# Kernel tuning notes

Measured on AMD Instinct MI355X. Metric: run time of the kernel, lower is better.

The kernel has to match this reference:

```python
import jax, jax.numpy as jnp
import numpy as np

N_HEAD = 16
NEG = -1e30  # finite stand-in for -inf; keeps softmax NaN-free


def setup_inputs() -> dict:
    key = jax.random.key(0)
    k1, k2, k3, k4, k5, k6 = jax.random.split(key, 6)
    B, T, C = 4, 2048, 1024
    x = jax.random.normal(k1, (B, T, C), dtype=jnp.float32)
    # realistic right-padding: True = padded position
    lengths = jax.random.randint(k2, (B,), T // 2, T + 1)  # at least half valid
    padding_mask = jnp.arange(T)[None, :] >= lengths[:, None]  # [B,T] bool
    s = 0.02
    W_attn = jax.random.normal(k3, (C, 3 * C), dtype=jnp.float32) * s
    b_attn = jnp.zeros((3 * C,), dtype=jnp.float32)
    W_proj = jax.random.normal(k4, (C, C), dtype=jnp.float32) * s
    b_proj = jnp.zeros((C,), dtype=jnp.float32)
    return {"x": x, "padding_mask": padding_mask, "W_attn": W_attn,
            "b_attn": b_attn, "W_proj": W_proj, "b_proj": b_proj}


def reference(x, padding_mask, W_attn, b_attn, W_proj, b_proj):
    B, T, C = x.shape
    H, D = N_HEAD, C // N_HEAD
    qkv = x @ W_attn + b_attn  # [B,T,3C]
    q, k, v = jnp.split(qkv, 3, axis=-1)
    q = q.reshape(B, T, H, D).transpose(0, 2, 1, 3)  # [B,H,T,D]
    k = k.reshape(B, T, H, D).transpose(0, 2, 1, 3)
    v = v.reshape(B, T, H, D).transpose(0, 2, 1, 3)
    att = jnp.einsum('bhqd,bhkd->bhqk', q, k) / jnp.sqrt(jnp.float32(D))
    causal = jnp.tril(jnp.ones((T, T), dtype=bool))  # [T,T]
    invalid = padding_mask[:, None, None, :] | ~causal[None, None]  # [B,1,T,T] key invalid
    att = jnp.where(invalid, NEG, att)
    att = jax.nn.softmax(att, axis=-1)
    # rows where every key is masked: torch softmax gives NaN -> nan_to_num(0)
    any_valid = jnp.any(~invalid, axis=-1, keepdims=True)  # [B,1,T,1]
    att = jnp.where(any_valid, att, 0.0)
    y = jnp.einsum('bhqk,bhkd->bhqd', att, v)  # [B,H,T,D]
    y = y.transpose(0, 2, 1, 3).reshape(B, T, C)
    y = y @ W_proj + b_proj
    y = jnp.where(padding_mask[:, :, None], 0.0, y)
    return y
```

## Files before the change

### kernel.cpp

```cpp
#include <hip/hip_runtime.h>
#include <stdint.h>

#define T_SEQ 2048
#define CDIM  1024
#define NH    16
#define DH    64
#define BATCH 4
#define MROWS (BATCH * T_SEQ)
#define N3    (3 * CDIM)
#define NEGBIG -1e30f

typedef unsigned short u16;
typedef __attribute__((ext_vector_type(8))) __bf16 bf16x8;
typedef __attribute__((ext_vector_type(4))) __bf16 bf16x4;
typedef __attribute__((ext_vector_type(8))) unsigned short u16x8;
typedef __attribute__((ext_vector_type(4))) float f32x4;
typedef __attribute__((ext_vector_type(16))) float f32x16;
typedef __attribute__((ext_vector_type(4))) unsigned int u32x4;

__device__ inline u16 f2bf(float f) {
  uint32_t u = __builtin_bit_cast(uint32_t, f);
  u += 0x7FFFu + ((u >> 16) & 1u);
  return (u16)(u >> 16);
}

__device__ inline void gld_lds16(const void* g, void* l) {
  __builtin_amdgcn_global_load_lds(
      (const __attribute__((address_space(1))) void*)g,
      (__attribute__((address_space(3))) void*)l, 16, 0, 0);
}


__global__ __launch_bounds__(256) void cvt_f32_bf16(
    const float* __restrict__ in, u16* __restrict__ out, int n) {
  int i = (blockIdx.x * 256 + threadIdx.x) * 4;
  if (i >= n) return;
  float4 v = *(const float4*)&in[i];
  ushort4 o; o.x = f2bf(v.x); o.y = f2bf(v.y); o.z = f2bf(v.z); o.w = f2bf(v.w);
  *(ushort4*)&out[i] = o;
}

__global__ __launch_bounds__(256) void wt_tiled(
    const float* __restrict__ W, u16* __restrict__ WT, int K, int N) {
  __shared__ float tile[64][65];
  const int k0 = blockIdx.y * 64, n0 = blockIdx.x * 64;
  const int t = threadIdx.x, cr = t >> 6, cc = t & 63;
#pragma unroll
  for (int i = 0; i < 16; i++) {
    int r = i * 4 + cr;
    tile[r][cc] = W[(size_t)(k0 + r) * N + n0 + cc];
  }
  __syncthreads();
#pragma unroll
  for (int i = 0; i < 16; i++) {
    int r = i * 4 + cr;
    WT[(size_t)(n0 + r) * K + k0 + cc] = f2bf(tile[cc][r]);
  }
}

__global__ __launch_bounds__(256) void len_kernel(
    const void* __restrict__ maskp, int* __restrict__ lengths) {
  __shared__ int flag;
  __shared__ int red[256];
  const int t = threadIdx.x, b = blockIdx.x;
  if (t == 0) flag = 0;
  __syncthreads();
  const uint32_t* mw = (const uint32_t*)maskp;
  int f = 0;
  for (int i = t; i < 2048; i += 256) f |= (mw[i] > 1u) ? 1 : 0;
  if (f) atomicOr(&flag, 1);
  __syncthreads();
  int cnt = 0;
  if (flag) {
    const uint8_t* mb = (const uint8_t*)maskp;
    for (int i = t; i < T_SEQ; i += 256) cnt += (mb[(size_t)b * T_SEQ + i] == 0);
  } else {
    const int* mi = (const int*)maskp;
    for (int i = t; i < T_SEQ; i += 256) cnt += (mi[(size_t)b * T_SEQ + i] == 0);
  }
  red[t] = cnt;
  __syncthreads();
  for (int s = 128; s > 0; s >>= 1) {
    if (t < s) red[t] += red[t + s];
    __syncthreads();
  }
  if (t == 0) lengths[b] = red[0];
}

template <int MODE>
__global__ __launch_bounds__(256, 2) void gemm_bf16(
    const u16* __restrict__ A, const u16* __restrict__ Bt,
    const float* __restrict__ bias,
    u16* __restrict__ Qb, u16* __restrict__ Kb, u16* __restrict__ Vt,
    float* __restrict__ Out, const int* __restrict__ lengths,
    int Mdim, int Ndim, int Kdim) {
  __shared__ u16 SM[16384];
  u16* As = SM;
  u16* Bs = SM + 8192;
  const int t = threadIdx.x;
  const int lane = t & 63, wid = t >> 6;
  const int wr = wid >> 1, wc = wid & 1;
  const int r16 = lane & 15, kg = lane >> 4;
  const int m0 = blockIdx.y * 128, n0 = blockIdx.x * 128;
  const int bb = m0 >> 11, tt0 = m0 & 2047;

  if (tt0 >= lengths[bb]) {
    if (MODE == 1) {
      const float4 z4 = make_float4(0.f, 0.f, 0.f, 0.f);
#pragma unroll
      for (int i = 0; i < 16; i++) {
        int u = i * 256 + t;
        int r = u >> 5, c4 = u & 31;
        *(float4*)&Out[(size_t)(m0 + r) * CDIM + n0 + c4 * 4] = z4;
      }
    }
    return;
  }

  f32x4 acc[4][4];
#pragma unroll
  for (int i = 0; i < 4; i++)
#pragma unroll
    for (int j = 0; j < 4; j++) acc[i][j] = (f32x4){0.f, 0.f, 0.f, 0.f};

  for (int k0 = 0; k0 < Kdim; k0 += 64) {
#pragma unroll
    for (int i = 0; i < 4; i++) {
      int idx = i * 256 + t;
      int row = idx >> 3;
      int chunk = idx & 7;
      int colel = (chunk * 8) ^ ((row & 7) << 3);
      gld_lds16(&A[(size_t)(m0 + row) * Kdim + k0 + colel], &As[idx * 8]);
      gld_lds16(&Bt[(size_t)(n0 + row) * Kdim + k0 + colel], &Bs[idx * 8]);
    }
    __syncthreads();

#pragma unroll
    for (int s = 0; s < 2; s++) {
      bf16x8 af[4], bfr[4];
#pragma unroll
      for (int m = 0; m < 4; m++) {
        int row = wr * 64 + m * 16 + r16;
        int colel = (s * 32 + kg * 8) ^ ((row & 7) << 3);
        af[m] = *(const bf16x8*)&As[row * 64 + colel];
      }
#pragma unroll
      for (int n = 0; n < 4; n++) {
        int row = wc * 64 + n * 16 + r16;
        int colel = (s * 32 + kg * 8) ^ ((row & 7) << 3);
        bfr[n] = *(const bf16x8*)&Bs[row * 64 + colel];
      }
#pragma unroll
      for (int m = 0; m < 4; m++)
#pragma unroll
        for (int n = 0; n < 4; n++)
          acc[m][n] = __builtin_amdgcn_mfma_f32_16x16x32_bf16(
              af[m], bfr[n], acc[m][n], 0, 0, 0);
    }
    __syncthreads();
  }

  if (MODE == 0) {
    const int b = bb;
    if (n0 >= 2048) {
      u16* Tt = SM;
#pragma unroll
      for (int m = 0; m < 4; m++)
#pragma unroll
        for (int n = 0; n < 4; n++) {
          int ln = wc * 64 + n * 16 + r16;
          float bv = bias[n0 + ln];
#pragma unroll
          for (int reg = 0; reg < 4; reg++) {
            int lm = wr * 64 + m * 16 + kg * 4 + reg;
            Tt[ln * 128 + (lm ^ ((ln & 7) << 3))] = f2bf(acc[m][n][reg] + bv);
          }
        }
      __syncthreads();
      const int cbase = n0 - 2048;
#pragma unroll
      for (int i = 0; i < 8; i++) {
        int u = i * 256 + t;
        int ln = u >> 4, ch = u & 15;
        u16x8 v = *(const u16x8*)&Tt[ln * 128 + ((ch * 8) ^ ((ln & 7) << 3))];
        int c = cbase + ln, hh = c >> 6, d = c & 63;
        *(u16x8*)&Vt[(((size_t)b * NH + hh) * DH + d) * T_SEQ + tt0 + ch * 8] = v;
      }
    } else {
      u16* Tt = SM;
#pragma unroll
      for (int m = 0; m < 4; m++)
#pragma unroll
        for (int n = 0; n < 4; n++) {
          int ln = wc * 64 + n * 16 + r16;
          float bv = bias[n0 + ln];
#pragma unroll
          for (int reg = 0; reg < 4; reg++) {
            int lm = wr * 64 + m * 16 + kg * 4 + reg;
            Tt[lm * 128 + (ln ^ ((lm & 7) << 3))] = f2bf(acc[m][n][reg] + bv);
          }
        }
      __syncthreads();
      const int cb = n0 & 1023;
      u16* dst = (n0 < 1024) ? Qb : Kb;
#pragma unroll
      for (int i = 0; i < 8; i++) {
        int u = i * 256 + t;
        int row = u >> 4, ch = u & 15;
        u16x8 v = *(const u16x8*)&Tt[row * 128 + ((ch * 8) ^ ((row & 7) << 3))];
        int c = cb + ch * 8, hh = c >> 6, d = c & 63;
        *(u16x8*)&dst[((size_t)(b * NH + hh) * T_SEQ + tt0 + row) * DH + d] = v;
      }
    }
    return;
  }

#pragma unroll
  for (int m = 0; m < 4; m++) {
    int gmb = m0 + wr * 64 + m * 16 + kg * 4;
#pragma unroll
    for (int n = 0; n < 4; n++) {
      int gn = n0 + wc * 64 + n * 16 + r16;
      float bv = bias[gn];
#pragma unroll
      for (int reg = 0; reg < 4; reg++) {
        float v = acc[m][n][reg] + bv;
        int row = gmb + reg;
        int b = row >> 11, tt = row & 2047;
        if (tt >= lengths[b]) v = 0.f;
        Out[(size_t)row * CDIM + gn] = v;
      }
    }
  }
}

__global__ __launch_bounds__(256) void attn32p_kernel(
    const u16* __restrict__ Qb, const u16* __restrict__ Kb,
    const u16* __restrict__ Vt, u16* __restrict__ yb,
    const int* __restrict__ lengths) {
  __shared__ __attribute__((aligned(16))) char smem[65536];
  const int t = threadIdx.x, lane = t & 63, wid = t >> 6;
  const int l31 = lane & 31, hi = lane >> 5;
  const int bh = blockIdx.y, b = bh >> 4, h = bh & (NH - 1);
  const int len = lengths[b];
  const int nAct = (len + 127) >> 7;
  const int npairs = (nAct + 1) >> 1;
  const int iq = blockIdx.x;
  if (iq >= npairs) return;
  const int q0L = iq * 128;
  const int q0H = (nAct - 1 - iq) * 128;
  const bool hiAct = q0H > q0L;
  const int q0Lw = q0L + wid * 32, q0Hw = q0H + wid * 32;
  const int qrowL = q0Lw + l31, qrowH = q0Hw + l31;
  const u16* Qh = Qb + (size_t)bh * T_SEQ * DH;
  const u16* Kh = Kb + (size_t)bh * T_SEQ * DH;
  const u16* Vth = Vt + (size_t)bh * DH * T_SEQ;
  const float SC = 0.18033688011112042f;
  const float THR = 44.3614195558365f;

  const int lenceil = (len + 63) & ~63;
  const int kvH = (q0H + 128 < lenceil) ? q0H + 128 : lenceil;
  const int kvL = (q0L + 128 < lenceil) ? q0L + 128 : lenceil;
  const int kv_end = hiAct ? kvH : kvL;
  const int ntiles = kv_end >> 6;

  bf16x8 qfL[4], qfH[4];
#pragma unroll
  for (int ks = 0; ks < 4; ks++) {
    qfL[ks] = *(const bf16x8*)&Qh[(size_t)qrowL * DH + ks * 16 + hi * 8];
    qfH[ks] = *(const bf16x8*)&Qh[(size_t)qrowH * DH + ks * 16 + hi * 8];
  }

  f32x16 oaccL[2], oaccH[2];
  oaccL[0] = (f32x16)0.f; oaccL[1] = (f32x16)0.f;
  oaccH[0] = (f32x16)0.f; oaccH[1] = (f32x16)0.f;
  float mL = NEGBIG, lL = 0.f, mH = NEGBIG, lH = 0.f;

  const int idx0 = t, idx1 = 256 + t;
  const int row0 = idx0 >> 3, ch0 = idx0 & 7;
  const int row1 = idx1 >> 3, ch1 = idx1 & 7;
  const int kc0 = (ch0 * 8) ^ ((row0 & 7) << 3);
  const int kc1 = (ch1 * 8) ^ ((row1 & 7) << 3);
  const char* kp0 = (const char*)Kh + ((size_t)row0 * DH + kc0) * 2;
  const char* kp1 = (const char*)Kh + ((size_t)row1 * DH + kc1) * 2;
  const char* vp0 = (const char*)Vth + ((size_t)row0 * T_SEQ + kc0) * 2;
  const char* vp1 = (const char*)Vth + ((size_t)row1 * T_SEQ + kc1) * 2;

  auto STAGE = [&](int bsel) {
    char* base = smem + bsel * 16384;
    gld_lds16(kp0, base + idx0 * 16);
    gld_lds16(kp1, base + idx1 * 16);
    gld_lds16(vp0, base + 8192 + idx0 * 16);
    gld_lds16(vp1, base + 8192 + idx1 * 16);
    kp0 += 8192; kp1 += 8192; vp0 += 128; vp1 += 128;
  };

  auto FLASH = [&](const u16* Ks, const u16* Vts, int kv0, int q0w, int qrow,
                   bf16x8* qf, f32x16* oacc, float& mrun, float& lrun) {
    f32x16 sacc[2];
    sacc[0] = (f32x16)0.f; sacc[1] = (f32x16)0.f;
#pragma unroll
    for (int kb = 0; kb < 2; kb++)
#pragma unroll
      for (int ks = 0; ks < 4; ks++) {
        int row = kb * 32 + l31;
        int col = (ks * 16 + hi * 8) ^ ((row & 7) << 3);
        bf16x8 ak = *(const bf16x8*)&Ks[row * 64 + col];
        sacc[kb] = __builtin_amdgcn_mfma_f32_32x32x16_bf16(
            ak, qf[ks], sacc[kb], 0, 0, 0);
      }

    if ((kv0 + 63 > q0w) || (kv0 + 64 > len)) {
#pragma unroll
      for (int kb = 0; kb < 2; kb++)
#pragma unroll
        for (int r = 0; r < 16; r++) {
          int key = kv0 + kb * 32 + (r & 3) + 8 * (r >> 2) + 4 * hi;
          if (key > qrow || key >= len) sacc[kb][r] = NEGBIG;
        }
    }
    float tm[16];
#pragma unroll
    for (int r = 0; r < 16; r++) tm[r] = fmaxf(sacc[0][r], sacc[1][r]);
#pragma unroll
    for (int r = 0; r < 8; r++) tm[r] = fmaxf(tm[r], tm[r + 8]);
#pragma unroll
    for (int r = 0; r < 4; r++) tm[r] = fmaxf(tm[r], tm[r + 4]);
    tm[0] = fmaxf(fmaxf(tm[0], tm[2]), fmaxf(tm[1], tm[3]));
    float mt = fmaxf(tm[0], __shfl_xor(tm[0], 32));

    if (!__all(mt <= mrun + THR)) {
      float mnew = fmaxf(mrun, mt);
      float fac = exp2f((mrun - mnew) * SC);
      mrun = mnew;
      lrun *= fac;
#pragma unroll
      for (int r = 0; r < 16; r++) { oacc[0][r] *= fac; oacc[1][r] *= fac; }
    }
    const float msc = mrun * SC;
#pragma unroll
    for (int kb = 0; kb < 2; kb++)
#pragma unroll
      for (int r = 0; r < 16; r++)
        sacc[kb][r] = exp2f(fmaf(sacc[kb][r], SC, -msc));
    float pt[16];
#pragma unroll
    for (int r = 0; r < 16; r++) pt[r] = sacc[0][r] + sacc[1][r];
#pragma unroll
    for (int r = 0; r < 8; r++) pt[r] += pt[r + 8];
#pragma unroll
    for (int r = 0; r < 4; r++) pt[r] += pt[r + 4];
    float ps = (pt[0] + pt[2]) + (pt[1] + pt[3]);
    ps += __shfl_xor(ps, 32);
    lrun += ps;

#pragma unroll
    for (int ks = 0; ks < 4; ks++) {
      const int kb = ks >> 1, rb = (ks & 1) * 8;
      uint32_t d0, d1, d2, d3;
      asm("v_cvt_pk_bf16_f32 %0, %1, %2" : "=v"(d0)
          : "v"(sacc[kb][rb + 0]), "v"(sacc[kb][rb + 1]));
      asm("v_cvt_pk_bf16_f32 %0, %1, %2" : "=v"(d1)
          : "v"(sacc[kb][rb + 2]), "v"(sacc[kb][rb + 3]));
      asm("v_cvt_pk_bf16_f32 %0, %1, %2" : "=v"(d2)
          : "v"(sacc[kb][rb + 4]), "v"(sacc[kb][rb + 5]));
      asm("v_cvt_pk_bf16_f32 %0, %1, %2" : "=v"(d3)
          : "v"(sacc[kb][rb + 6]), "v"(sacc[kb][rb + 7]));
      bf16x8 pb = __builtin_bit_cast(bf16x8, (u32x4){d0, d1, d2, d3});
#pragma unroll
      for (int mb = 0; mb < 2; mb++) {
        int row = mb * 32 + l31;
        int sw = (row & 7);
        bf16x4 v1 = *(const bf16x4*)&Vts[row * 64 + ((2 * ks) ^ sw) * 8 + 4 * hi];
        bf16x4 v2 = *(const bf16x4*)&Vts[row * 64 + ((2 * ks + 1) ^ sw) * 8 + 4 * hi];
        bf16x8 av;
#pragma unroll
        for (int j = 0; j < 4; j++) { av[j] = v1[j]; av[4 + j] = v2[j]; }
        oacc[mb] = __builtin_amdgcn_mfma_f32_32x32x16_bf16(
            av, pb, oacc[mb], 0, 0, 0);
      }
    }
  };

  STAGE(0); STAGE(1);
  for (int it = 0; it < ntiles; ++it) {
    if (it + 2 < ntiles) STAGE((it + 2) & 3);
    const int r = ntiles - 1 - it;
    if (r >= 2)      asm volatile("s_waitcnt vmcnt(8)" ::: "memory");
    else if (r == 1) asm volatile("s_waitcnt vmcnt(4)" ::: "memory");
    else             asm volatile("s_waitcnt vmcnt(0)" ::: "memory");
    __builtin_amdgcn_s_barrier();
    __builtin_amdgcn_sched_barrier(0);

    const u16* Ks  = (const u16*)(smem + (it & 3) * 16384);
    const u16* Vts = (const u16*)(smem + (it & 3) * 16384 + 8192);
    const int kv0 = it << 6;
    if (hiAct && kv0 <= q0Hw + 31)
      FLASH(Ks, Vts, kv0, q0Hw, qrowH, qfH, oaccH, mH, lH);
    if (kv0 <= q0Lw + 31)
      FLASH(Ks, Vts, kv0, q0Lw, qrowL, qfL, oaccL, mL, lL);
  }
  __syncthreads();

  u16* yt = (u16*)smem + wid * (32 * 72);
  auto EPI = [&](f32x16* oacc, float lrun, int q0w) {
    const float inv = (lrun > 0.f) ? 1.f / lrun : 0.f;
#pragma unroll
    for (int mb = 0; mb < 2; mb++)
#pragma unroll
      for (int r = 0; r < 16; r += 2) {
        int d = mb * 32 + (r & 3) + 8 * (r >> 2) + 4 * hi;
        float a0 = oacc[mb][r] * inv, a1 = oacc[mb][r + 1] * inv;
        uint32_t pw;
        asm("v_cvt_pk_bf16_f32 %0, %1, %2" : "=v"(pw) : "v"(a0), "v"(a1));
        *(uint32_t*)&yt[l31 * 72 + d] = pw;
      }
    asm volatile("s_waitcnt lgkmcnt(0)" ::: "memory");
    __builtin_amdgcn_sched_barrier(0);
#pragma unroll
    for (int pass = 0; pass < 4; pass++) {
      int rowq = pass * 8 + (lane >> 3);
      int col8 = (lane & 7) * 8;
      u16x8 v = *(const u16x8*)&yt[rowq * 72 + col8];
      *(u16x8*)&yb[((size_t)b * T_SEQ + q0w + rowq) * CDIM + h * DH + col8] = v;
    }
    asm volatile("s_waitcnt lgkmcnt(0)" ::: "memory");
    __builtin_amdgcn_sched_barrier(0);
  };
  EPI(oaccL, lL, q0Lw);
  if (hiAct) EPI(oaccH, lH, q0Hw);
}

extern "C" void kernel_launch(void* const* d_in, const int* in_sizes, int n_in,
                              void* d_out, int out_size, void* d_ws, size_t ws_size,
                              hipStream_t stream) {
  const float* x  = (const float*)d_in[0];
  const void*  mask = d_in[1];
  const float* Wa = (const float*)d_in[2];
  const float* ba = (const float*)d_in[3];
  const float* Wp = (const float*)d_in[4];
  const float* bp = (const float*)d_in[5];
  float* out = (float*)d_out;

  char* w = (char*)d_ws;
  u16* xb  = (u16*)w; w += (size_t)MROWS * CDIM * 2;
  u16* WaT = (u16*)w; w += (size_t)N3 * CDIM * 2;
  u16* WpT = (u16*)w; w += (size_t)CDIM * CDIM * 2;
  u16* Qb  = (u16*)w; w += (size_t)MROWS * CDIM * 2;
  u16* Kb  = (u16*)w; w += (size_t)MROWS * CDIM * 2;
  u16* Vt  = (u16*)w; w += (size_t)MROWS * CDIM * 2;
  int* lengths = (int*)w;
  u16* yb = xb;

  cvt_f32_bf16<<<(MROWS * CDIM / 4 + 255) / 256, 256, 0, stream>>>(x, xb, MROWS * CDIM);
  wt_tiled<<<dim3(N3 / 64, CDIM / 64), 256, 0, stream>>>(Wa, WaT, CDIM, N3);
  wt_tiled<<<dim3(CDIM / 64, CDIM / 64), 256, 0, stream>>>(Wp, WpT, CDIM, CDIM);
  len_kernel<<<BATCH, 256, 0, stream>>>(mask, lengths);

  gemm_bf16<0><<<dim3(N3 / 128, MROWS / 128), 256, 0, stream>>>(
      xb, WaT, ba, Qb, Kb, Vt, nullptr, lengths, MROWS, N3, CDIM);

  attn32p_kernel<<<dim3(8, BATCH * NH), 256, 0, stream>>>(
      Qb, Kb, Vt, yb, lengths);

  gemm_bf16<1><<<dim3(CDIM / 128, MROWS / 128), 256, 0, stream>>>(
      yb, WpT, bp, nullptr, nullptr, nullptr, out, lengths, MROWS, CDIM, CDIM);
}
```

Baseline: 229.9 us.

## Add 256x256 double-buffered QKV GEMM with 8 waves and MFMA priority

Replaces the QKV projection GEMM with a dedicated kernel that uses 256x256 output tiles, 512 threads and a double-buffered 128KB LDS stage. The next K-tile's global-to-LDS loads overlap the current tile's MFMAs, and s_setprio is raised around the MFMA bursts. The goal is more data reuse per tile and hidden load latency. The cost is heavy LDS use, which allows only one block per CU, fewer blocks overall (wave quantization on 256 CUs), and coarser padding skip at 256-row granularity.

```diff
diff --git a/kernel.cpp b/kernel.cpp
--- a/kernel.cpp
+++ b/kernel.cpp
@@ -87,13 +87,149 @@
   if (t == 0) lengths[b] = red[0];
 }
 
-template <int MODE>
-__global__ __launch_bounds__(256, 2) void gemm_bf16(
+__global__ __launch_bounds__(512, 2) void gemm256_qkv(
     const u16* __restrict__ A, const u16* __restrict__ Bt,
     const float* __restrict__ bias,
     u16* __restrict__ Qb, u16* __restrict__ Kb, u16* __restrict__ Vt,
-    float* __restrict__ Out, const int* __restrict__ lengths,
-    int Mdim, int Ndim, int Kdim) {
+    const int* __restrict__ lengths) {
+  __shared__ __attribute__((aligned(16))) char smem[131072];
+  const int t = threadIdx.x;
+  const int lane = t & 63, wid = t >> 6;
+  const int wm = wid >> 2, wn = wid & 3;
+  const int r16 = lane & 15, kg = lane >> 4;
+  const int m0 = blockIdx.y * 256, n0 = blockIdx.x * 256;
+  const int b = m0 >> 11, tt0 = m0 & 2047;
+  if (tt0 >= lengths[b]) return;
+
+  f32x4 acc[8][4];
+#pragma unroll
+  for (int i = 0; i < 8; i++)
+#pragma unroll
+    for (int j = 0; j < 4; j++) acc[i][j] = (f32x4){0.f, 0.f, 0.f, 0.f};
+
+  auto STAGE_TILE = [&](int buf, int kt) {
+    const int k0 = kt * 64;
+    char* Ad = smem + buf * 32768;
+    char* Bd = smem + 65536 + buf * 32768;
+#pragma unroll
+    for (int i = 0; i < 4; i++) {
+      int c = i * 512 + t;
+      int row = c >> 3, ch = c & 7;
+      int col = (ch * 8) ^ ((row & 7) << 3);
+      gld_lds16(&A[(size_t)(m0 + row) * CDIM + k0 + col], Ad + c * 16);
+      gld_lds16(&Bt[(size_t)(n0 + row) * CDIM + k0 + col], Bd + c * 16);
+    }
+  };
+
+  STAGE_TILE(0, 0);
+  for (int it = 0; it < 16; ++it) {
+    if (it + 1 < 16) {
+      STAGE_TILE((it + 1) & 1, it + 1);
+      asm volatile("s_waitcnt vmcnt(8)" ::: "memory");
+    } else {
+      asm volatile("s_waitcnt vmcnt(0)" ::: "memory");
+    }
+    __builtin_amdgcn_s_barrier();
+
+    const u16* Ar = (const u16*)(smem + (it & 1) * 32768);
+    const u16* Br = (const u16*)(smem + 65536 + (it & 1) * 32768);
+#pragma unroll
+    for (int p = 0; p < 4; p++) {
+      const int qm = p >> 1, qn = p & 1;
+      bf16x8 af[4][2], bfr[2][2];
+#pragma unroll
+      for (int mi = 0; mi < 4; mi++)
+#pragma unroll
+        for (int s = 0; s < 2; s++) {
+          int row = wm * 128 + (qm * 4 + mi) * 16 + r16;
+          int col = (s * 32 + kg * 8) ^ ((row & 7) << 3);
+          af[mi][s] = *(const bf16x8*)&Ar[row * 64 + col];
+        }
+#pragma unroll
+      for (int ni = 0; ni < 2; ni++)
+#pragma unroll
+        for (int s = 0; s < 2; s++) {
+          int row = wn * 64 + (qn * 2 + ni) * 16 + r16;
+          int col = (s * 32 + kg * 8) ^ ((row & 7) << 3);
+          bfr[ni][s] = *(const bf16x8*)&Br[row * 64 + col];
+        }
+      __builtin_amdgcn_s_barrier();
+      asm volatile("s_waitcnt lgkmcnt(0)" ::: "memory");
+      __builtin_amdgcn_sched_barrier(0);
+      __builtin_amdgcn_s_setprio(1);
+#pragma unroll
+      for (int s = 0; s < 2; s++)
+#pragma unroll
+        for (int mi = 0; mi < 4; mi++)
+#pragma unroll
+          for (int ni = 0; ni < 2; ni++)
+            acc[qm * 4 + mi][qn * 2 + ni] =
+                __builtin_amdgcn_mfma_f32_16x16x32_bf16(
+                    af[mi][s], bfr[ni][s], acc[qm * 4 + mi][qn * 2 + ni],
+                    0, 0, 0);
+      __builtin_amdgcn_s_setprio(0);
+      __builtin_amdgcn_s_barrier();
+    }
+  }
+  __syncthreads();
+
+  u16* Tt = (u16*)smem;
+  if (n0 >= 2048) {
+#pragma unroll
+    for (int m = 0; m < 8; m++)
+#pragma unroll
+      for (int n = 0; n < 4; n++) {
+        int ln = wn * 64 + n * 16 + r16;
+        float bv = bias[n0 + ln];
+        int lmb = wm * 128 + m * 16 + kg * 4;
+        ushort4 pk;
+        pk.x = f2bf(acc[m][n][0] + bv);
+        pk.y = f2bf(acc[m][n][1] + bv);
+        pk.z = f2bf(acc[m][n][2] + bv);
+        pk.w = f2bf(acc[m][n][3] + bv);
+        *(ushort4*)&Tt[ln * 256 + (lmb ^ ((ln & 7) << 3))] = pk;
+      }
+    __syncthreads();
+    const int cbase = n0 - 2048;
+#pragma unroll
+    for (int i = 0; i < 16; i++) {
+      int u = i * 512 + t;
+      int ln = u >> 5, ch = u & 31;
+      u16x8 v = *(const u16x8*)&Tt[ln * 256 + ((ch * 8) ^ ((ln & 7) << 3))];
+      int c = cbase + ln, hh = c >> 6, d = c & 63;
+      *(u16x8*)&Vt[(((size_t)b * NH + hh) * DH + d) * T_SEQ + tt0 + ch * 8] = v;
+    }
+  } else {
+#pragma unroll
+    for (int m = 0; m < 8; m++)
+#pragma unroll
+      for (int n = 0; n < 4; n++) {
+        int ln = wn * 64 + n * 16 + r16;
+        float bv = bias[n0 + ln];
+#pragma unroll
+        for (int reg = 0; reg < 4; reg++) {
+          int lm = wm * 128 + m * 16 + kg * 4 + reg;
+          Tt[lm * 256 + (ln ^ ((lm & 7) << 3))] = f2bf(acc[m][n][reg] + bv);
+        }
+      }
+    __syncthreads();
+    const int cb = n0 & 1023;
+    u16* dst = (n0 < 1024) ? Qb : Kb;
+#pragma unroll
+    for (int i = 0; i < 16; i++) {
+      int u = i * 512 + t;
+      int row = u >> 5, ch = u & 31;
+      u16x8 v = *(const u16x8*)&Tt[row * 256 + ((ch * 8) ^ ((row & 7) << 3))];
+      int c = cb + ch * 8, hh = c >> 6, d = c & 63;
+      *(u16x8*)&dst[((size_t)(b * NH + hh) * T_SEQ + tt0 + row) * DH + d] = v;
+    }
+  }
+}
+
+__global__ __launch_bounds__(256, 2) void gemm_proj(
+    const u16* __restrict__ A, const u16* __restrict__ Bt,
+    const float* __restrict__ bias,
+    float* __restrict__ Out, const int* __restrict__ lengths, int Kdim) {
   __shared__ u16 SM[16384];
   u16* As = SM;
   u16* Bs = SM + 8192;
@@ -105,14 +241,12 @@
   const int bb = m0 >> 11, tt0 = m0 & 2047;
 
   if (tt0 >= lengths[bb]) {
-    if (MODE == 1) {
-      const float4 z4 = make_float4(0.f, 0.f, 0.f, 0.f);
-#pragma unroll
-      for (int i = 0; i < 16; i++) {
-        int u = i * 256 + t;
-        int r = u >> 5, c4 = u & 31;
-        *(float4*)&Out[(size_t)(m0 + r) * CDIM + n0 + c4 * 4] = z4;
-      }
+    const float4 z4 = make_float4(0.f, 0.f, 0.f, 0.f);
+#pragma unroll
+    for (int i = 0; i < 16; i++) {
+      int u = i * 256 + t;
+      int r = u >> 5, c4 = u & 31;
+      *(float4*)&Out[(size_t)(m0 + r) * CDIM + n0 + c4 * 4] = z4;
     }
     return;
   }
@@ -158,61 +292,6 @@
               af[m], bfr[n], acc[m][n], 0, 0, 0);
     }
     __syncthreads();
-  }
-
-  if (MODE == 0) {
-    const int b = bb;
-    if (n0 >= 2048) {
-      u16* Tt = SM;
-#pragma unroll
-      for (int m = 0; m < 4; m++)
-#pragma unroll
-        for (int n = 0; n < 4; n++) {
-          int ln = wc * 64 + n * 16 + r16;
-          float bv = bias[n0 + ln];
-#pragma unroll
-          for (int reg = 0; reg < 4; reg++) {
-            int lm = wr * 64 + m * 16 + kg * 4 + reg;
-            Tt[ln * 128 + (lm ^ ((ln & 7) << 3))] = f2bf(acc[m][n][reg] + bv);
-          }
-        }
-      __syncthreads();
-      const int cbase = n0 - 2048;
-#pragma unroll
-      for (int i = 0; i < 8; i++) {
-        int u = i * 256 + t;
-        int ln = u >> 4, ch = u & 15;
-        u16x8 v = *(const u16x8*)&Tt[ln * 128 + ((ch * 8) ^ ((ln & 7) << 3))];
-        int c = cbase + ln, hh = c >> 6, d = c & 63;
-        *(u16x8*)&Vt[(((size_t)b * NH + hh) * DH + d) * T_SEQ + tt0 + ch * 8] = v;
-      }
-    } else {
-      u16* Tt = SM;
-#pragma unroll
-      for (int m = 0; m < 4; m++)
-#pragma unroll
-        for (int n = 0; n < 4; n++) {
-          int ln = wc * 64 + n * 16 + r16;
-          float bv = bias[n0 + ln];
-#pragma unroll
-          for (int reg = 0; reg < 4; reg++) {
-            int lm = wr * 64 + m * 16 + kg * 4 + reg;
-            Tt[lm * 128 + (ln ^ ((lm & 7) << 3))] = f2bf(acc[m][n][reg] + bv);
-          }
-        }
-      __syncthreads();
-      const int cb = n0 & 1023;
-      u16* dst = (n0 < 1024) ? Qb : Kb;
-#pragma unroll
-      for (int i = 0; i < 8; i++) {
-        int u = i * 256 + t;
-        int row = u >> 4, ch = u & 15;
-        u16x8 v = *(const u16x8*)&Tt[row * 128 + ((ch * 8) ^ ((row & 7) << 3))];
-        int c = cb + ch * 8, hh = c >> 6, d = c & 63;
-        *(u16x8*)&dst[((size_t)(b * NH + hh) * T_SEQ + tt0 + row) * DH + d] = v;
-      }
-    }
-    return;
   }
 
 #pragma unroll
@@ -457,12 +536,12 @@
   wt_tiled<<<dim3(CDIM / 64, CDIM / 64), 256, 0, stream>>>(Wp, WpT, CDIM, CDIM);
   len_kernel<<<BATCH, 256, 0, stream>>>(mask, lengths);
 
-  gemm_bf16<0><<<dim3(N3 / 128, MROWS / 128), 256, 0, stream>>>(
-      xb, WaT, ba, Qb, Kb, Vt, nullptr, lengths, MROWS, N3, CDIM);
+  gemm256_qkv<<<dim3(N3 / 256, MROWS / 256), 512, 0, stream>>>(
+      xb, WaT, ba, Qb, Kb, Vt, lengths);
 
   attn32p_kernel<<<dim3(8, BATCH * NH), 256, 0, stream>>>(
       Qb, Kb, Vt, yb, lengths);
 
-  gemm_bf16<1><<<dim3(CDIM / 128, MROWS / 128), 256, 0, stream>>>(
-      yb, WpT, bp, nullptr, nullptr, nullptr, out, lengths, MROWS, CDIM, CDIM);
-}
+  gemm_proj<<<dim3(CDIM / 128, MROWS / 128), 256, 0, stream>>>(
+      yb, WpT, bp, out, lengths, CDIM);
+}
```

Measured after the change: 241.5 us. +5.1%, slower.
